# Optimization experiments

Measured on AMD Instinct MI355X. Metric: run time of the kernel, lower is better.

## Reference

```python
import jax, jax.numpy as jnp
import numpy as np

ATTR_LEN = [2, 4, 4, 2, 6]
CUM = np.concatenate(([0], np.cumsum(ATTR_LEN)))  # [0,2,6,10,12,18]
B, S, D, V = 4096, 200, 64, 100000


def setup_inputs() -> dict:
    key = jax.random.key(0)
    ks = jax.random.split(key, 10)
    x = jax.random.randint(ks[0], (B, S), 0, V)
    # one-hot labels per attribute, concatenated -> [B, 18]
    y_parts = []
    for i, al in enumerate(ATTR_LEN):
        lab = jax.random.randint(jax.random.fold_in(ks[1], i), (B,), 0, al)
        y_parts.append(jax.nn.one_hot(lab, al, dtype=jnp.float32))
    y = jnp.concatenate(y_parts, axis=1)
    emb_table = jax.random.normal(ks[2], (V, D), jnp.float32) * 0.02
    emb_table = emb_table.at[0].set(0.0)  # padding_idx=0
    att_w = jax.random.normal(ks[3], (5, D), jnp.float32) * 0.1
    att_b = jax.random.normal(ks[4], (5,), jnp.float32) * 0.1
    W0 = jax.random.normal(ks[5], (ATTR_LEN[0], D), jnp.float32) * 0.1
    W1 = jax.random.normal(ks[6], (ATTR_LEN[1], D), jnp.float32) * 0.1
    W2 = jax.random.normal(ks[7], (ATTR_LEN[2], D), jnp.float32) * 0.1
    W3 = jax.random.normal(ks[8], (ATTR_LEN[3], D), jnp.float32) * 0.1
    W4 = jax.random.normal(ks[9], (ATTR_LEN[4], D), jnp.float32) * 0.1
    return {"x": x, "y": y, "emb_table": emb_table, "att_w": att_w,
            "att_b": att_b, "W0": W0, "W1": W1, "W2": W2, "W3": W3, "W4": W4}


def reference(x, y, emb_table, att_w, att_b, W0, W1, W2, W3, W4):
    embed = emb_table[x]  # [B, S, D] gather (padding row is zero)
    # 5 per-attribute additive tanh-attention heads, batched over k.
    # Softmax over seq axis is independent per head, so stacking is exact.
    att_u = jnp.tanh(jnp.einsum('bsd,kd->bsk', embed, att_w) + att_b)  # [B,S,5]
    score = jax.nn.softmax(att_u, axis=1)                              # [B,S,5]
    user_rep = jnp.einsum('bsd,bsk->bkd', embed, score)                # [B,5,D]
    Ws = [W0, W1, W2, W3, W4]
    # per-task bias-free linear heads, concatenated -> [B, 18]
    W_user = jnp.concatenate([user_rep[:, i] @ Ws[i].T for i in range(5)], axis=1)
    logits = []
    loss = jnp.float32(0.0)
    for i in range(5):
        Wc = W_user[:, CUM[i]:CUM[i + 1]]
        yc = y[:, CUM[i]:CUM[i + 1]]
        # partial_training=False -> ob = ones -> all rows kept;
        # obj = exp(sum(W*y)) / sum_j exp(W_j)  ==  softmax picked at label
        logp = jax.nn.log_softmax(Wc, axis=1)
        loss = loss + (-jnp.sum(logp * yc) / Wc.shape[0])
        logits.append(jax.nn.softmax(Wc, axis=1))
    logit = jnp.concatenate(logits, axis=1)  # [B, 18]
    return logit, loss
```

## Files before the change

kernel.cpp:

```cpp
#include <hip/hip_runtime.h>
#include <math.h>

#define Bsz 4096
#define Ssz 200
#define Dsz 64
#define NK  5
#define NT  512
#define ROWH 72
#define AWS  72

typedef _Float16 half_t;
typedef _Float16 h2 __attribute__((ext_vector_type(2)));
typedef _Float16 h8 __attribute__((ext_vector_type(8)));
typedef float    f4v __attribute__((ext_vector_type(4)));

__device__ inline h2 shfl_xor_h2(h2 v, int m) {
    int iv = __builtin_bit_cast(int, v);
    iv = __shfl_xor(iv, m);
    return __builtin_bit_cast(h2, iv);
}

__global__ void zero_loss_kernel(float* loss) {
    if (threadIdx.x == 0) *loss = 0.0f;
}

__global__ __launch_bounds__(NT, 8) void tan_kernel(
    const int* __restrict__ x, const float* __restrict__ y,
    const float* __restrict__ emb_table,
    const float* __restrict__ att_w, const float* __restrict__ att_b,
    const float* __restrict__ W0, const float* __restrict__ W1,
    const float* __restrict__ W2, const float* __restrict__ W3,
    const float* __restrict__ W4,
    float* __restrict__ out_logit, float* __restrict__ loss_out)
{
    __shared__ alignas(16) half_t embh[208 * ROWH];
    __shared__ alignas(16) half_t att_h[NK][208];
    __shared__ alignas(16) half_t aw_h[16 * AWS];
    __shared__ alignas(16) half_t urph[8][NK][Dsz];
    __shared__ alignas(16) int    xs[Ssz];
    __shared__ float wu[18];

    const int b   = blockIdx.x;
    const int tid = threadIdx.x;
    const int w   = tid >> 6;
    const int l   = tid & 63;

    if (tid < Ssz) xs[tid] = x[b * Ssz + tid];
    for (int i = tid; i < 1024; i += NT)
        aw_h[(i >> 6) * AWS + (i & 63)] =
            ((i >> 6) < NK) ? (half_t)att_w[i] : (half_t)0;
    {
        uint4 zz = {0, 0, 0, 0};
        uint4* zp = (uint4*)(embh + 200 * ROWH);
        for (int i = tid; i < 72; i += NT) zp[i] = zz;
    }
    __syncthreads();

    {
        float4 v[7];
#pragma unroll
        for (int p = 0; p < 7; ++p) {
            int i = tid + NT * p;
            if (i > Ssz * 16 - 1) i = Ssz * 16 - 1;
            const int s = i >> 4, c = i & 15;
            v[p] = ((const float4*)(emb_table + (size_t)xs[s] * Dsz))[c];
        }
#pragma unroll
        for (int p = 0; p < 7; ++p) {
            const int i = tid + NT * p;
            if (p < 6 || i < Ssz * 16) {
                const int s = i >> 4, c = i & 15;
                h2 a  = (h2){(half_t)v[p].x, (half_t)v[p].y};
                h2 b2 = (h2){(half_t)v[p].z, (half_t)v[p].w};
                uint2 u = { __builtin_bit_cast(unsigned, a),
                            __builtin_bit_cast(unsigned, b2) };
                *(uint2*)(embh + s * ROWH + c * 4) = u;
            }
        }
    }
    __syncthreads();

    {
        const int lm = l & 15;
        const int lq = l >> 4;
        h8 a0 = *(const h8*)(aw_h + lm * AWS + lq * 8);
        h8 a1 = *(const h8*)(aw_h + lm * AWS + lq * 8 + 32);
        for (int t = w; t < 13; t += 8) {
            const int s = t * 16 + lm;
            h8 b0 = *(const h8*)(embh + s * ROWH + lq * 8);
            h8 b1 = *(const h8*)(embh + s * ROWH + lq * 8 + 32);
            f4v acc = {0.f, 0.f, 0.f, 0.f};
            acc = __builtin_amdgcn_mfma_f32_16x16x32_f16(a0, b0, acc, 0, 0, 0);
            acc = __builtin_amdgcn_mfma_f32_16x16x32_f16(a1, b1, acc, 0, 0, 0);
#pragma unroll
            for (int r = 0; r < 4; ++r) {
                const int k = lq * 4 + r;
                if (k < NK)
                    att_h[k][s] = (half_t)tanhf(acc[r] + att_b[k]);
            }
        }
    }
    __syncthreads();

    if (w < NK) {
        const int k = w;
        float vals[4];
        float mx = -1e30f;
#pragma unroll
        for (int j = 0; j < 4; ++j) {
            int s = l + 64 * j;
            vals[j] = (s < Ssz) ? (float)att_h[k][s] : -1e30f;
            mx = fmaxf(mx, vals[j]);
        }
#pragma unroll
        for (int m = 32; m >= 1; m >>= 1) mx = fmaxf(mx, __shfl_xor(mx, m));
        float sum = 0.f;
#pragma unroll
        for (int j = 0; j < 4; ++j) {
            vals[j] = __expf(vals[j] - mx);
            sum += vals[j];
        }
#pragma unroll
        for (int m = 32; m >= 1; m >>= 1) sum += __shfl_xor(sum, m);
        float inv = 1.0f / sum;
#pragma unroll
        for (int j = 0; j < 4; ++j) {
            int s = l + 64 * j;
            if (s < Ssz) att_h[k][s] = (half_t)(vals[j] * inv);
        }
    }
    __syncthreads();

    {
        const int c = tid & 15;
        const int j = tid >> 4;
        h2 acc[NK][2];
#pragma unroll
        for (int k = 0; k < NK; ++k)
#pragma unroll
            for (int i = 0; i < 2; ++i) acc[k][i] = (h2){(half_t)0, (half_t)0};
#pragma unroll
        for (int t = 0; t < 7; ++t) {
            const int s = j + 32 * t;
            if (s < Ssz) {
                union { uint2 q; h2 hh[2]; } u;
                u.q = *(const uint2*)(embh + s * ROWH + c * 4);
#pragma unroll
                for (int k = 0; k < NK; ++k) {
                    half_t f = att_h[k][s];
                    h2 sc = (h2){f, f};
                    acc[k][0] += u.hh[0] * sc;
                    acc[k][1] += u.hh[1] * sc;
                }
            }
        }
#pragma unroll
        for (int k = 0; k < NK; ++k)
#pragma unroll
            for (int i = 0; i < 2; ++i) {
                acc[k][i] += shfl_xor_h2(acc[k][i], 16);
                acc[k][i] += shfl_xor_h2(acc[k][i], 32);
            }
        if (l < 16) {
#pragma unroll
            for (int k = 0; k < NK; ++k) {
                union { h2 a[2]; uint2 q; } uu;
                uu.a[0] = acc[k][0]; uu.a[1] = acc[k][1];
                *(uint2*)(&urph[w][k][l * 4]) = uu.q;
            }
        }
    }
    __syncthreads();

    for (int j = w; j < 18; j += 8) {
        const float* Wp; int g, c0;
        if      (j < 2)  { g = 0; c0 = 0;  Wp = W0; }
        else if (j < 6)  { g = 1; c0 = 2;  Wp = W1; }
        else if (j < 10) { g = 2; c0 = 6;  Wp = W2; }
        else if (j < 12) { g = 3; c0 = 10; Wp = W3; }
        else             { g = 4; c0 = 12; Wp = W4; }
        float urv = 0.f;
#pragma unroll
        for (int jj = 0; jj < 8; ++jj) urv += (float)urph[jj][g][l];
        float p = urv * Wp[(j - c0) * Dsz + l];
#pragma unroll
        for (int m = 32; m >= 1; m >>= 1) p += __shfl_xor(p, m);
        if (l == 0) wu[j] = p;
    }
    __syncthreads();

    if (w == 0) {
        float lossb = 0.f;
        if (l < NK) {
            const int LEN[5] = {2, 4, 4, 2, 6};
            const int C0[5]  = {0, 2, 6, 10, 12};
            const int g = l, c0 = C0[g], len = LEN[g];
            float* op = out_logit + (size_t)b * 18;
            const float* yp = y + (size_t)b * 18;
            float mx = -1e30f;
            for (int j = 0; j < len; ++j) mx = fmaxf(mx, wu[c0 + j]);
            float sum = 0.f;
            for (int j = 0; j < len; ++j) sum += __expf(wu[c0 + j] - mx);
            float inv = 1.0f / sum;
            float lse = mx + __logf(sum);
            for (int j = 0; j < len; ++j) {
                op[c0 + j] = __expf(wu[c0 + j] - mx) * inv;
                lossb += (lse - wu[c0 + j]) * yp[c0 + j];
            }
        }
#pragma unroll
        for (int m = 1; m <= 4; m <<= 1) lossb += __shfl_xor(lossb, m);
        if (l == 0) atomicAdd(loss_out, lossb * (1.0f / Bsz));
    }
}

extern "C" void kernel_launch(void* const* d_in, const int* in_sizes, int n_in,
                              void* d_out, int out_size, void* d_ws, size_t ws_size,
                              hipStream_t stream) {
    const int*   x   = (const int*)d_in[0];
    const float* y   = (const float*)d_in[1];
    const float* emb = (const float*)d_in[2];
    const float* aw  = (const float*)d_in[3];
    const float* ab  = (const float*)d_in[4];
    const float* W0  = (const float*)d_in[5];
    const float* W1  = (const float*)d_in[6];
    const float* W2  = (const float*)d_in[7];
    const float* W3  = (const float*)d_in[8];
    const float* W4  = (const float*)d_in[9];
    float* out  = (float*)d_out;
    float* loss = out + (size_t)Bsz * 18;

    zero_loss_kernel<<<1, 64, 0, stream>>>(loss);
    tan_kernel<<<Bsz, NT, 0, stream>>>(x, y, emb, aw, ab,
                                       W0, W1, W2, W3, W4, out, loss);
}
```

Measured before the change: 156.8 us.

## Fuse embedding gather into MFMA stage with swizzled LDS layout and fast tanh

The embedding gather now goes straight from global memory into MFMA B fragments, and the same fragments are then written to LDS in an XOR-swizzled layout. This removes the separate gather/convert pass and two barriers, and the attention weights are loaded directly into registers instead of through LDS. Tanh is replaced by an exp-based formula, and the weighted-sum stage gives each thread 8 consecutive positions with vectorized score loads. The risk is less memory-level parallelism, since the gather is split over only 13 tiles across 8 waves with serialized loop iterations, and a small accuracy change from the approximate tanh.

```diff
diff --git a/kernel.cpp b/kernel.cpp
--- a/kernel.cpp
+++ b/kernel.cpp
@@ -6,8 +6,8 @@
 #define Dsz 64
 #define NK  5
 #define NT  512
-#define ROWH 72
-#define AWS  72
+#define ROWH 80
+#define ATS 208
 
 typedef _Float16 half_t;
 typedef _Float16 h2 __attribute__((ext_vector_type(2)));
@@ -18,6 +18,16 @@
     int iv = __builtin_bit_cast(int, v);
     iv = __shfl_xor(iv, m);
     return __builtin_bit_cast(h2, iv);
+}
+
+__device__ inline h2 pk(float a, float b) {
+    return __builtin_bit_cast(h2, __builtin_amdgcn_cvt_pkrtz(a, b));
+}
+
+__device__ inline float fast_tanh(float x) {
+    float e = __expf(-2.0f * fabsf(x));
+    float r = (1.0f - e) / (1.0f + e);
+    return copysignf(r, x);
 }
 
 __global__ void zero_loss_kernel(float* loss) {
@@ -34,69 +44,62 @@
     float* __restrict__ out_logit, float* __restrict__ loss_out)
 {
     __shared__ alignas(16) half_t embh[208 * ROWH];
-    __shared__ alignas(16) half_t att_h[NK][208];
-    __shared__ alignas(16) half_t aw_h[16 * AWS];
+    __shared__ alignas(16) half_t att_h[NK * ATS];
     __shared__ alignas(16) half_t urph[8][NK][Dsz];
-    __shared__ alignas(16) int    xs[Ssz];
     __shared__ float wu[18];
 
     const int b   = blockIdx.x;
     const int tid = threadIdx.x;
     const int w   = tid >> 6;
     const int l   = tid & 63;
-
-    if (tid < Ssz) xs[tid] = x[b * Ssz + tid];
-    for (int i = tid; i < 1024; i += NT)
-        aw_h[(i >> 6) * AWS + (i & 63)] =
-            ((i >> 6) < NK) ? (half_t)att_w[i] : (half_t)0;
+    const int lm  = l & 15;
+    const int lq  = l >> 4;
+
     {
-        uint4 zz = {0, 0, 0, 0};
-        uint4* zp = (uint4*)(embh + 200 * ROWH);
-        for (int i = tid; i < 72; i += NT) zp[i] = zz;
-    }
-    __syncthreads();
-
-    {
-        float4 v[7];
-#pragma unroll
-        for (int p = 0; p < 7; ++p) {
-            int i = tid + NT * p;
-            if (i > Ssz * 16 - 1) i = Ssz * 16 - 1;
-            const int s = i >> 4, c = i & 15;
-            v[p] = ((const float4*)(emb_table + (size_t)xs[s] * Dsz))[c];
-        }
-#pragma unroll
-        for (int p = 0; p < 7; ++p) {
-            const int i = tid + NT * p;
-            if (p < 6 || i < Ssz * 16) {
-                const int s = i >> 4, c = i & 15;
-                h2 a  = (h2){(half_t)v[p].x, (half_t)v[p].y};
-                h2 b2 = (h2){(half_t)v[p].z, (half_t)v[p].w};
-                uint2 u = { __builtin_bit_cast(unsigned, a),
-                            __builtin_bit_cast(unsigned, b2) };
-                *(uint2*)(embh + s * ROWH + c * 4) = u;
-            }
-        }
-    }
-    __syncthreads();
-
-    {
-        const int lm = l & 15;
-        const int lq = l >> 4;
-        h8 a0 = *(const h8*)(aw_h + lm * AWS + lq * 8);
-        h8 a1 = *(const h8*)(aw_h + lm * AWS + lq * 8 + 32);
+        h8 afrag[2];
+#pragma unroll
+        for (int st = 0; st < 2; ++st) {
+            if (lm < NK) {
+                const float4* ap = (const float4*)(att_w + lm * Dsz + 32 * st + 8 * lq);
+                float4 a0 = ap[0], a1 = ap[1];
+                union { h2 hh[4]; h8 v; } ua;
+                ua.hh[0] = pk(a0.x, a0.y); ua.hh[1] = pk(a0.z, a0.w);
+                ua.hh[2] = pk(a1.x, a1.y); ua.hh[3] = pk(a1.z, a1.w);
+                afrag[st] = ua.v;
+            } else {
+                afrag[st] = (h8)(half_t)0;
+            }
+        }
         for (int t = w; t < 13; t += 8) {
-            const int s = t * 16 + lm;
-            h8 b0 = *(const h8*)(embh + s * ROWH + lq * 8);
-            h8 b1 = *(const h8*)(embh + s * ROWH + lq * 8 + 32);
+            const int s  = 16 * t + lm;
+            const int sc = (s < Ssz) ? s : (Ssz - 1);
+            const int xi = x[b * Ssz + sc];
+            const float* rowp = emb_table + (size_t)xi * Dsz;
+            h8 bfr[2];
+#pragma unroll
+            for (int st = 0; st < 2; ++st) {
+                const float4* bp = (const float4*)(rowp + 32 * st + 8 * lq);
+                float4 b0 = bp[0], b1 = bp[1];
+                union { h2 hh[4]; h8 v; } ub;
+                ub.hh[0] = pk(b0.x, b0.y); ub.hh[1] = pk(b0.z, b0.w);
+                ub.hh[2] = pk(b1.x, b1.y); ub.hh[3] = pk(b1.z, b1.w);
+                bfr[st] = ub.v;
+            }
             f4v acc = {0.f, 0.f, 0.f, 0.f};
-            acc = __builtin_amdgcn_mfma_f32_16x16x32_f16(a0, b0, acc, 0, 0, 0);
-            acc = __builtin_amdgcn_mfma_f32_16x16x32_f16(a1, b1, acc, 0, 0, 0);
+            acc = __builtin_amdgcn_mfma_f32_16x16x32_f16(afrag[0], bfr[0], acc, 0, 0, 0);
+            acc = __builtin_amdgcn_mfma_f32_16x16x32_f16(afrag[1], bfr[1], acc, 0, 0, 0);
+            const int js = (s >> 3) & 7;
+#pragma unroll
+            for (int st = 0; st < 2; ++st) {
+                const int gp = (4 * st + lq) ^ js;
+                *(h8*)(embh + s * ROWH + gp * 8) = bfr[st];
+            }
 #pragma unroll
             for (int r = 0; r < 4; ++r) {
                 const int k = lq * 4 + r;
                 if (k < NK)
-                    att_h[k][s] = (half_t)tanhf(acc[r] + att_b[k]);
+                    att_h[k * ATS + 16 * t + lm] =
+                        (half_t)fast_tanh(acc[r] + att_b[k]);
             }
         }
     }
@@ -109,7 +112,7 @@
 #pragma unroll
         for (int j = 0; j < 4; ++j) {
             int s = l + 64 * j;
-            vals[j] = (s < Ssz) ? (float)att_h[k][s] : -1e30f;
+            vals[j] = (s < Ssz) ? (float)att_h[k * ATS + s] : -1e30f;
             mx = fmaxf(mx, vals[j]);
         }
 #pragma unroll
@@ -126,7 +129,7 @@
 #pragma unroll
         for (int j = 0; j < 4; ++j) {
             int s = l + 64 * j;
-            if (s < Ssz) att_h[k][s] = (half_t)(vals[j] * inv);
+            if (s < Ssz) att_h[k * ATS + s] = (half_t)(vals[j] * inv);
         }
     }
     __syncthreads();
@@ -134,38 +137,45 @@
     {
         const int c = tid & 15;
         const int j = tid >> 4;
-        h2 acc[NK][2];
-#pragma unroll
-        for (int k = 0; k < NK; ++k)
-#pragma unroll
-            for (int i = 0; i < 2; ++i) acc[k][i] = (h2){(half_t)0, (half_t)0};
-#pragma unroll
-        for (int t = 0; t < 7; ++t) {
-            const int s = j + 32 * t;
-            if (s < Ssz) {
-                union { uint2 q; h2 hh[2]; } u;
-                u.q = *(const uint2*)(embh + s * ROWH + c * 4);
+        h2 acc0[NK], acc1[NK];
+#pragma unroll
+        for (int k = 0; k < NK; ++k) {
+            acc0[k] = (h2){(half_t)0, (half_t)0};
+            acc1[k] = (h2){(half_t)0, (half_t)0};
+        }
+        if (j < 25) {
+            union { h8 v; h2 hh[4]; } sc[NK];
+#pragma unroll
+            for (int k = 0; k < NK; ++k)
+                sc[k].v = *(const h8*)(att_h + k * ATS + 8 * j);
+            const int gp = (c >> 1) ^ (j & 7);
+            const int sub = (c & 1) * 4;
+#pragma unroll
+            for (int i = 0; i < 8; ++i) {
+                const int s = 8 * j + i;
+                union { uint2 q; h2 hh[2]; } ue;
+                ue.q = *(const uint2*)(embh + s * ROWH + gp * 8 + sub);
 #pragma unroll
                 for (int k = 0; k < NK; ++k) {
-                    half_t f = att_h[k][s];
-                    h2 sc = (h2){f, f};
-                    acc[k][0] += u.hh[0] * sc;
-                    acc[k][1] += u.hh[1] * sc;
+                    half_t f = sc[k].hh[i >> 1][i & 1];
+                    h2 s2 = (h2){f, f};
+                    acc0[k] += ue.hh[0] * s2;
+                    acc1[k] += ue.hh[1] * s2;
                 }
             }
         }
 #pragma unroll
-        for (int k = 0; k < NK; ++k)
-#pragma unroll
-            for (int i = 0; i < 2; ++i) {
-                acc[k][i] += shfl_xor_h2(acc[k][i], 16);
-                acc[k][i] += shfl_xor_h2(acc[k][i], 32);
-            }
+        for (int k = 0; k < NK; ++k) {
+            acc0[k] += shfl_xor_h2(acc0[k], 16);
+            acc0[k] += shfl_xor_h2(acc0[k], 32);
+            acc1[k] += shfl_xor_h2(acc1[k], 16);
+            acc1[k] += shfl_xor_h2(acc1[k], 32);
+        }
         if (l < 16) {
 #pragma unroll
             for (int k = 0; k < NK; ++k) {
                 union { h2 a[2]; uint2 q; } uu;
-                uu.a[0] = acc[k][0]; uu.a[1] = acc[k][1];
+                uu.a[0] = acc0[k]; uu.a[1] = acc1[k];
                 *(uint2*)(&urph[w][k][l * 4]) = uu.q;
             }
         }
```

Result: slower. 161.8 us (+3.2%).

## Use MFMA for attention-weighted pooling and streamline embedding/attention setup

Applied to the files above, without the earlier changes.

Replaces the packed-half FMA pooling loop (and its cross-lane shuffles) with 16x16x32 MFMA ops. Score tiles act as A and embedding columns as B, split over 8 waves by 16-column d-slice and sequence half. It also drops the xs/aw_h shared staging, loading token ids and attention weights straight from global memory into registers. Scores stay in fp32 shared memory with a fast exp-based tanh, and fp16 conversion uses cvt_pkrtz. The B operand is gathered element-wise with strided LDS reads, which may cause bank conflicts, and round-toward-zero conversion slightly changes numerics.

```diff
diff --git a/kernel.cpp b/kernel.cpp
--- a/kernel.cpp
+++ b/kernel.cpp
@@ -7,17 +7,21 @@
 #define NK  5
 #define NT  512
 #define ROWH 72
-#define AWS  72
+#define SA  224
 
 typedef _Float16 half_t;
 typedef _Float16 h2 __attribute__((ext_vector_type(2)));
 typedef _Float16 h8 __attribute__((ext_vector_type(8)));
 typedef float    f4v __attribute__((ext_vector_type(4)));
 
-__device__ inline h2 shfl_xor_h2(h2 v, int m) {
-    int iv = __builtin_bit_cast(int, v);
-    iv = __shfl_xor(iv, m);
-    return __builtin_bit_cast(h2, iv);
+__device__ inline h2 pk(float a, float b) {
+    return __builtin_bit_cast(h2, __builtin_amdgcn_cvt_pkrtz(a, b));
+}
+
+__device__ inline float fast_tanh(float x) {
+    float e = __expf(-2.0f * fabsf(x));
+    float r = (1.0f - e) / (1.0f + e);
+    return copysignf(r, x);
 }
 
 __global__ void zero_loss_kernel(float* loss) {
@@ -33,47 +37,45 @@
     const float* __restrict__ W4,
     float* __restrict__ out_logit, float* __restrict__ loss_out)
 {
-    __shared__ alignas(16) half_t embh[208 * ROWH];
-    __shared__ alignas(16) half_t att_h[NK][208];
-    __shared__ alignas(16) half_t aw_h[16 * AWS];
-    __shared__ alignas(16) half_t urph[8][NK][Dsz];
-    __shared__ alignas(16) int    xs[Ssz];
+    __shared__ alignas(16) half_t embh[224 * ROWH];
+    __shared__ alignas(16) float  att[NK][Ssz];
+    __shared__ alignas(16) half_t att_hf[NK * SA];
+    __shared__ alignas(16) half_t urph[2][NK][Dsz];
     __shared__ float wu[18];
 
     const int b   = blockIdx.x;
     const int tid = threadIdx.x;
     const int w   = tid >> 6;
     const int l   = tid & 63;
-
-    if (tid < Ssz) xs[tid] = x[b * Ssz + tid];
-    for (int i = tid; i < 1024; i += NT)
-        aw_h[(i >> 6) * AWS + (i & 63)] =
-            ((i >> 6) < NK) ? (half_t)att_w[i] : (half_t)0;
+    const int lm  = l & 15;
+    const int lq  = l >> 4;
+
     {
         uint4 zz = {0, 0, 0, 0};
         uint4* zp = (uint4*)(embh + 200 * ROWH);
-        for (int i = tid; i < 72; i += NT) zp[i] = zz;
-    }
-    __syncthreads();
-
-    {
+        for (int i = tid; i < 216; i += NT) zp[i] = zz;
+    }
+
+    {
+        const int* xb = x + b * Ssz;
         float4 v[7];
 #pragma unroll
         for (int p = 0; p < 7; ++p) {
             int i = tid + NT * p;
             if (i > Ssz * 16 - 1) i = Ssz * 16 - 1;
             const int s = i >> 4, c = i & 15;
-            v[p] = ((const float4*)(emb_table + (size_t)xs[s] * Dsz))[c];
+            const int xi = xb[s];
+            v[p] = ((const float4*)(emb_table + (size_t)xi * Dsz))[c];
         }
 #pragma unroll
         for (int p = 0; p < 7; ++p) {
             const int i = tid + NT * p;
             if (p < 6 || i < Ssz * 16) {
                 const int s = i >> 4, c = i & 15;
-                h2 a  = (h2){(half_t)v[p].x, (half_t)v[p].y};
-                h2 b2 = (h2){(half_t)v[p].z, (half_t)v[p].w};
-                uint2 u = { __builtin_bit_cast(unsigned, a),
-                            __builtin_bit_cast(unsigned, b2) };
+                h2 lo = pk(v[p].x, v[p].y);
+                h2 hi = pk(v[p].z, v[p].w);
+                uint2 u = { __builtin_bit_cast(unsigned, lo),
+                            __builtin_bit_cast(unsigned, hi) };
                 *(uint2*)(embh + s * ROWH + c * 4) = u;
             }
         }
@@ -81,22 +83,33 @@
     __syncthreads();
 
     {
-        const int lm = l & 15;
-        const int lq = l >> 4;
-        h8 a0 = *(const h8*)(aw_h + lm * AWS + lq * 8);
-        h8 a1 = *(const h8*)(aw_h + lm * AWS + lq * 8 + 32);
+        h8 afrag[2];
+#pragma unroll
+        for (int st = 0; st < 2; ++st) {
+            if (lm < NK) {
+                const float4* ap = (const float4*)(att_w + lm * Dsz + 32 * st + 8 * lq);
+                float4 a0 = ap[0], a1 = ap[1];
+                union { h2 hh[4]; h8 v; } ua;
+                ua.hh[0] = pk(a0.x, a0.y); ua.hh[1] = pk(a0.z, a0.w);
+                ua.hh[2] = pk(a1.x, a1.y); ua.hh[3] = pk(a1.z, a1.w);
+                afrag[st] = ua.v;
+            } else {
+                afrag[st] = (h8)(half_t)0;
+            }
+        }
         for (int t = w; t < 13; t += 8) {
-            const int s = t * 16 + lm;
-            h8 b0 = *(const h8*)(embh + s * ROWH + lq * 8);
-            h8 b1 = *(const h8*)(embh + s * ROWH + lq * 8 + 32);
+            const int s = 16 * t + lm;
+            h8 b0 = *(const h8*)(embh + s * ROWH + 8 * lq);
+            h8 b1 = *(const h8*)(embh + s * ROWH + 32 + 8 * lq);
             f4v acc = {0.f, 0.f, 0.f, 0.f};
-            acc = __builtin_amdgcn_mfma_f32_16x16x32_f16(a0, b0, acc, 0, 0, 0);
-            acc = __builtin_amdgcn_mfma_f32_16x16x32_f16(a1, b1, acc, 0, 0, 0);
+            acc = __builtin_amdgcn_mfma_f32_16x16x32_f16(afrag[0], b0, acc, 0, 0, 0);
+            acc = __builtin_amdgcn_mfma_f32_16x16x32_f16(afrag[1], b1, acc, 0, 0, 0);
+            const int sc = 16 * t + lm;
 #pragma unroll
             for (int r = 0; r < 4; ++r) {
                 const int k = lq * 4 + r;
-                if (k < NK)
-                    att_h[k][s] = (half_t)tanhf(acc[r] + att_b[k]);
+                if (k < NK && sc < Ssz)
+                    att[k][sc] = fast_tanh(acc[r] + att_b[k]);
             }
         }
     }
@@ -109,7 +122,7 @@
 #pragma unroll
         for (int j = 0; j < 4; ++j) {
             int s = l + 64 * j;
-            vals[j] = (s < Ssz) ? (float)att_h[k][s] : -1e30f;
+            vals[j] = (s < Ssz) ? att[k][s] : -1e30f;
             mx = fmaxf(mx, vals[j]);
         }
 #pragma unroll
@@ -126,48 +139,35 @@
 #pragma unroll
         for (int j = 0; j < 4; ++j) {
             int s = l + 64 * j;
-            if (s < Ssz) att_h[k][s] = (half_t)(vals[j] * inv);
-        }
-    }
-    __syncthreads();
-
-    {
-        const int c = tid & 15;
-        const int j = tid >> 4;
-        h2 acc[NK][2];
-#pragma unroll
-        for (int k = 0; k < NK; ++k)
-#pragma unroll
-            for (int i = 0; i < 2; ++i) acc[k][i] = (h2){(half_t)0, (half_t)0};
-#pragma unroll
-        for (int t = 0; t < 7; ++t) {
-            const int s = j + 32 * t;
-            if (s < Ssz) {
-                union { uint2 q; h2 hh[2]; } u;
-                u.q = *(const uint2*)(embh + s * ROWH + c * 4);
-#pragma unroll
-                for (int k = 0; k < NK; ++k) {
-                    half_t f = att_h[k][s];
-                    h2 sc = (h2){f, f};
-                    acc[k][0] += u.hh[0] * sc;
-                    acc[k][1] += u.hh[1] * sc;
-                }
-            }
-        }
-#pragma unroll
-        for (int k = 0; k < NK; ++k)
-#pragma unroll
-            for (int i = 0; i < 2; ++i) {
-                acc[k][i] += shfl_xor_h2(acc[k][i], 16);
-                acc[k][i] += shfl_xor_h2(acc[k][i], 32);
-            }
-        if (l < 16) {
-#pragma unroll
-            for (int k = 0; k < NK; ++k) {
-                union { h2 a[2]; uint2 q; } uu;
-                uu.a[0] = acc[k][0]; uu.a[1] = acc[k][1];
-                *(uint2*)(&urph[w][k][l * 4]) = uu.q;
-            }
+            if (s < Ssz)            att_hf[k * SA + s] = (half_t)(vals[j] * inv);
+            else if (s < SA)        att_hf[k * SA + s] = (half_t)0;
+        }
+    }
+    __syncthreads();
+
+    {
+        const int d0 = (w & 3) * 16;
+        const int hh = w >> 2;
+        const int nst   = hh ? 3 : 4;
+        const int sbase = hh ? 128 : 0;
+        f4v acc = {0.f, 0.f, 0.f, 0.f};
+        for (int st = 0; st < nst; ++st) {
+            const int s0 = sbase + 32 * st;
+            h8 afr;
+            if (lm < NK) afr = *(const h8*)(att_hf + lm * SA + s0 + lq * 8);
+            else         afr = (h8)(half_t)0;
+            union { h8 v; half_t e[8]; } ub;
+#pragma unroll
+            for (int j = 0; j < 8; ++j)
+                ub.e[j] = embh[(s0 + lq * 8 + j) * ROWH + d0 + lm];
+            acc = __builtin_amdgcn_mfma_f32_16x16x32_f16(afr, ub.v, acc, 0, 0, 0);
+        }
+        if (lq == 0) {
+#pragma unroll
+            for (int r = 0; r < 4; ++r)
+                urph[hh][r][d0 + lm] = (half_t)acc[r];
+        } else if (lq == 1) {
+            urph[hh][4][d0 + lm] = (half_t)acc[0];
         }
     }
     __syncthreads();
@@ -179,9 +179,7 @@
         else if (j < 10) { g = 2; c0 = 6;  Wp = W2; }
         else if (j < 12) { g = 3; c0 = 10; Wp = W3; }
         else             { g = 4; c0 = 12; Wp = W4; }
-        float urv = 0.f;
-#pragma unroll
-        for (int jj = 0; jj < 8; ++jj) urv += (float)urph[jj][g][l];
+        float urv = (float)urph[0][g][l] + (float)urph[1][g][l];
         float p = urv * Wp[(j - c0) * Dsz + l];
 #pragma unroll
         for (int m = 32; m >= 1; m >>= 1) p += __shfl_xor(p, m);
```

After: 159.5 us. Within noise of the previous version (+1.7%).
